# Optimization experiments

Hardware: AMD Instinct MI355X
Metric: run time of the kernel (lower is better)

Reference implementation:

```python
import jax, jax.numpy as jnp
import numpy as np
from jax import lax

H, W = 64, 64          # image_shape grid
TOP_K = 3
N_ITER = 50
EPS = 1e-8
NPTS = 3072            # N = M feature points (<= H*W)
SQRT2 = 1.4142135623730951
INV_SQRT3 = 1.0 / 1.7320508075688772


def setup_inputs() -> dict:
    key = jax.random.key(0)
    P = jax.random.uniform(key, (NPTS + 1, NPTS + 1), dtype=jnp.float32)
    K = jnp.array([[500.0, 0.0, 320.0],
                   [0.0, 500.0, 240.0],
                   [0.0, 0.0, 1.0]], dtype=jnp.float32)
    return {"P": P, "K": K}


def _power_iter(Mm, v0):
    # n_iter steps of v <- Mm @ v / ||.||  (differentiable via scan)
    def step(v, _):
        v = Mm @ v
        return v / (jnp.linalg.norm(v) + EPS), None
    v, _ = lax.scan(step, v0, None, length=N_ITER)
    return v


def _det3(M):
    return (M[0, 0] * (M[1, 1] * M[2, 2] - M[1, 2] * M[2, 1])
            - M[0, 1] * (M[1, 0] * M[2, 2] - M[1, 2] * M[2, 0])
            + M[0, 2] * (M[1, 0] * M[2, 1] - M[1, 1] * M[2, 0]))


def _hartley(pts, w):
    # weighted centroid + scale so weighted RMS distance = sqrt(2)
    ws = w.sum() + EPS
    c = (w[:, None] * pts).sum(0) / ws
    pc = pts - c
    md = jnp.sqrt((w * (pc ** 2).sum(-1)).sum() / ws + EPS)
    s = jnp.asarray(SQRT2, pts.dtype) / (md + EPS)
    z = jnp.zeros((), pts.dtype)
    o = jnp.ones((), pts.dtype)
    T = jnp.stack([jnp.stack([s, z, -s * c[0]]),
                   jnp.stack([z, s, -s * c[1]]),
                   jnp.stack([z, z, o])])
    return T, s, c


def _project_E(E):
    # project onto essential manifold: singular values -> [s, s, 0]
    B = E.T @ E
    lam = jnp.trace(B)
    v0 = jnp.full((3,), INV_SQRT3, E.dtype)
    v1 = _power_iter(B, v0)                                   # max eigvec of E^T E
    v3 = _power_iter(lam * jnp.eye(3, dtype=E.dtype) - B, v0)  # min eigvec
    v2 = jnp.cross(v3, v1)
    v2 = v2 / (jnp.linalg.norm(v2) + EPS)
    V = jnp.stack([v1, v2, v3], axis=-1)
    one = jnp.ones((), E.dtype)
    sV = jnp.sign(_det3(V))
    V = V * jnp.stack([one, one, sV])[None, :]
    Ev1 = E @ V[:, 0]
    Ev2 = E @ V[:, 1]
    s1 = jnp.linalg.norm(Ev1)
    s2 = jnp.linalg.norm(Ev2)
    s_avg = (s1 + s2) / 2.0
    u1 = Ev1 / (s1 + EPS)
    u2 = Ev2 / (s2 + EPS)
    u3 = jnp.cross(u1, u2)
    U = jnp.stack([u1, u2, u3], axis=-1)
    sU = jnp.sign(_det3(U))
    U = U * jnp.stack([one, one, sU])[None, :]
    z = jnp.zeros((), E.dtype)
    # U @ diag(s_avg, s_avg, 0) @ V^T, diag folded into column scaling
    return (U * jnp.stack([s_avg, s_avg, z])[None, :]) @ V.T


def reference(P, K):
    N = P.shape[0] - 1
    M = P.shape[1] - 1
    Pc = P[:N, :M]
    # bidirectional top-k + absolute threshold
    tr = lax.top_k(Pc, TOP_K)[0][:, TOP_K - 1]          # (N,) row thresholds
    tc = lax.top_k(Pc.T, TOP_K)[0][:, TOP_K - 1]        # (M,) col thresholds
    mask = (Pc >= tr[:, None]) & (Pc >= tc[None, :]) & (Pc > 0.01)
    weights = Pc * mask.astype(Pc.dtype)
    # grid pixel coords -> normalized camera coords via K^-1
    idx = jnp.arange(H * W, dtype=Pc.dtype)
    pix = jnp.stack([idx % W, jnp.floor(idx / W)], axis=-1)  # (HW, 2)
    K_inv = jnp.linalg.inv(K)
    p1h = jnp.concatenate([pix[:N], jnp.ones((N, 1), Pc.dtype)], axis=-1)
    p2h = jnp.concatenate([pix[:M], jnp.ones((M, 1), Pc.dtype)], axis=-1)
    pts1 = (p1h @ K_inv.T)[:, :2]
    pts2 = (p2h @ K_inv.T)[:, :2]
    w1 = weights.sum(1)
    w2 = weights.sum(0)
    T1, s1, c1 = _hartley(pts1, w1)
    T2, s2, c2 = _hartley(pts2, w2)
    p1 = (pts1 - c1) * s1
    p2 = (pts2 - c2) * s2
    x1, y1 = p1[:, 0], p1[:, 1]
    x2, y2 = p2[:, 0], p2[:, 1]
    on = jnp.ones((N,), Pc.dtype)
    om = jnp.ones((M,), Pc.dtype)
    # (N, M, 9) epipolar design matrix
    A = jnp.stack([x1[:, None] * x2[None, :], x1[:, None] * y2[None, :], x1[:, None] * om[None, :],
                   y1[:, None] * x2[None, :], y1[:, None] * y2[None, :], y1[:, None] * om[None, :],
                   on[:, None] * x2[None, :], on[:, None] * y2[None, :], jnp.ones((N, M), Pc.dtype)],
                  axis=-1)
    A9 = A.reshape(N * M, 9)
    Mmat = (A9 * weights.reshape(-1, 1)).T @ A9            # 9x9 weighted Gram
    # min eigenvector via shifted power iteration
    lam = jnp.trace(Mmat)
    Ms = lam * jnp.eye(9, dtype=Mmat.dtype) - Mmat
    v = _power_iter(Ms, jnp.full((9,), 1.0 / 3.0, Mmat.dtype))
    E_raw = v.reshape(3, 3)
    E = T2.T @ E_raw @ T1                                   # Hartley denormalize
    return _project_E(E)
```

## Files before the change

### kernel.cpp

```cpp
#include <hip/hip_runtime.h>
#include <math.h>

#define NPV 3072
#define LDP 3073
#define EPSF 1e-8f
#define NMOM 52
#define NROWBLK (NPV / 64)

#define INS3(v, a, b, c) do { \
    float _m1 = fminf((a), (v)); (a) = fmaxf((a), (v)); \
    float _m2 = fminf((b), _m1); (b) = fmaxf((b), _m1); \
    (c) = fmaxf((c), _m2); } while (0)

#define MRG3(x, y, z, a, b, c) do { \
    INS3((x), a, b, c); INS3((y), a, b, c); INS3((z), a, b, c); } while (0)

__device__ __forceinline__ void kinv6(const float* __restrict__ Kmat,
        float& ki0, float& ki1, float& ki2, float& ki3, float& ki4, float& ki5)
{
    float k00 = Kmat[0], k01 = Kmat[1], k02 = Kmat[2];
    float k10 = Kmat[3], k11 = Kmat[4], k12 = Kmat[5];
    float k20 = Kmat[6], k21 = Kmat[7], k22 = Kmat[8];
    float det = k00 * (k11 * k22 - k12 * k21) - k01 * (k10 * k22 - k12 * k20) + k02 * (k10 * k21 - k11 * k20);
    float id = 1.0f / det;
    ki0 = (k11 * k22 - k12 * k21) * id; ki1 = (k02 * k21 - k01 * k22) * id; ki2 = (k01 * k12 - k02 * k11) * id;
    ki3 = (k12 * k20 - k10 * k22) * id; ki4 = (k00 * k22 - k02 * k20) * id; ki5 = (k02 * k10 - k00 * k12) * id;
}

__global__ __launch_bounds__(256) void k_row_top3(const float* __restrict__ P,
        float* __restrict__ tr, int* __restrict__ rowcnt)
{
    int lane = threadIdx.x & 63;
    int i = blockIdx.x * 4 + (threadIdx.x >> 6);
    const float* row = P + (size_t)i * LDP;
    float a0 = -1e30f, b0 = -1e30f, c0 = -1e30f;
    float a1 = -1e30f, b1 = -1e30f, c1 = -1e30f;
    float a2 = -1e30f, b2 = -1e30f, c2 = -1e30f;
    float a3 = -1e30f, b3 = -1e30f, c3 = -1e30f;
    #pragma unroll
    for (int r = 0; r < 48; r += 4) {
        float v0 = row[(r + 0) * 64 + lane];
        float v1 = row[(r + 1) * 64 + lane];
        float v2 = row[(r + 2) * 64 + lane];
        float v3 = row[(r + 3) * 64 + lane];
        INS3(v0, a0, b0, c0);
        INS3(v1, a1, b1, c1);
        INS3(v2, a2, b2, c2);
        INS3(v3, a3, b3, c3);
    }
    MRG3(a1, b1, c1, a0, b0, c0);
    MRG3(a2, b2, c2, a0, b0, c0);
    MRG3(a3, b3, c3, a0, b0, c0);
    #pragma unroll
    for (int off = 1; off < 64; off <<= 1) {
        float xa = __shfl_xor(a0, off);
        float xb = __shfl_xor(b0, off);
        float xc = __shfl_xor(c0, off);
        MRG3(xa, xb, xc, a0, b0, c0);
    }
    if (lane == 0) { tr[i] = c0; rowcnt[i] = 0; }
}

#define CAND(v, i) do { \
    if ((v) >= tr[i] && (v) > 0.01f) { \
        int _s = atomicAdd(&rowcnt[i], 1); \
        if (_s < 8) { rowj[(size_t)(i) * 8 + _s] = j; roww[(size_t)(i) * 8 + _s] = (v); } \
    } } while (0)

__global__ __launch_bounds__(256) void k_col_pass(const float* __restrict__ P,
        const float* __restrict__ tr, float4* __restrict__ part, int segrows,
        int* __restrict__ rowcnt, int* __restrict__ rowj, float* __restrict__ roww)
{
    int j = blockIdx.x * 256 + threadIdx.x;
    int i0 = blockIdx.y * segrows;
    float a0 = -1e30f, b0 = -1e30f, c0 = -1e30f;
    float a1 = -1e30f, b1 = -1e30f, c1 = -1e30f;
    float a2 = -1e30f, b2 = -1e30f, c2 = -1e30f;
    float a3 = -1e30f, b3 = -1e30f, c3 = -1e30f;
    float a4 = -1e30f, b4 = -1e30f, c4 = -1e30f;
    float a5 = -1e30f, b5 = -1e30f, c5 = -1e30f;
    float a6 = -1e30f, b6 = -1e30f, c6 = -1e30f;
    float a7 = -1e30f, b7 = -1e30f, c7 = -1e30f;
    for (int r = 0; r < segrows; r += 8) {
        int i = i0 + r;
        const float* col = P + (size_t)i * LDP + j;
        float v0 = col[0 * LDP];
        float v1 = col[1 * LDP];
        float v2 = col[2 * LDP];
        float v3 = col[3 * LDP];
        float v4 = col[4 * LDP];
        float v5 = col[5 * LDP];
        float v6 = col[6 * LDP];
        float v7 = col[7 * LDP];
        INS3(v0, a0, b0, c0);
        INS3(v1, a1, b1, c1);
        INS3(v2, a2, b2, c2);
        INS3(v3, a3, b3, c3);
        INS3(v4, a4, b4, c4);
        INS3(v5, a5, b5, c5);
        INS3(v6, a6, b6, c6);
        INS3(v7, a7, b7, c7);
        CAND(v0, i + 0);
        CAND(v1, i + 1);
        CAND(v2, i + 2);
        CAND(v3, i + 3);
        CAND(v4, i + 4);
        CAND(v5, i + 5);
        CAND(v6, i + 6);
        CAND(v7, i + 7);
    }
    MRG3(a1, b1, c1, a0, b0, c0);
    MRG3(a2, b2, c2, a0, b0, c0);
    MRG3(a3, b3, c3, a0, b0, c0);
    MRG3(a4, b4, c4, a0, b0, c0);
    MRG3(a5, b5, c5, a0, b0, c0);
    MRG3(a6, b6, c6, a0, b0, c0);
    MRG3(a7, b7, c7, a0, b0, c0);
    part[(size_t)blockIdx.y * NPV + j] = make_float4(a0, b0, c0, 0.f);
}

template<int NSEG>
__global__ __launch_bounds__(256) void k_col_merge(const float4* __restrict__ part,
        float* __restrict__ tc)
{
    int sub = threadIdx.x & 15;
    int j = blockIdx.x * 16 + (threadIdx.x >> 4);
    constexpr int CNT = NSEG / 16;
    float4 buf[CNT];
    #pragma unroll
    for (int k = 0; k < CNT; ++k)
        buf[k] = part[(size_t)(sub + (k << 4)) * NPV + j];
    float a = -1e30f, b = -1e30f, c = -1e30f;
    #pragma unroll
    for (int k = 0; k < CNT; ++k) MRG3(buf[k].x, buf[k].y, buf[k].z, a, b, c);
    #pragma unroll
    for (int off = 1; off < 16; off <<= 1) {
        float xa = __shfl_xor(a, off);
        float xb = __shfl_xor(b, off);
        float xc = __shfl_xor(c, off);
        MRG3(xa, xb, xc, a, b, c);
    }
    if (sub == 0) tc[j] = c;
}

__device__ __forceinline__ void acc_pair(float* m, float w, float xs1, float ys1,
                                         float xs2, float ys2)
{
    m[0] += w;
    m[1] += w * xs1; m[2] += w * ys1; m[3] += w * (xs1 * xs1 + ys1 * ys1);
    m[4] += w * xs2; m[5] += w * ys2; m[6] += w * (xs2 * xs2 + ys2 * ys2);
    float a[9] = { xs1 * xs2, xs1 * ys2, xs1, ys1 * xs2, ys1 * ys2, ys1, xs2, ys2, 1.f };
    int idx = 7;
    #pragma unroll
    for (int u = 0; u < 9; ++u) {
        float wa = w * a[u];
        #pragma unroll
        for (int v = u; v < 9; ++v) { m[idx] = fmaf(wa, a[v], m[idx]); ++idx; }
    }
}

__global__ __launch_bounds__(64) void k_moments(const float* __restrict__ Kmat,
        const float* __restrict__ tc, const int* __restrict__ rowcnt,
        const int* __restrict__ rowj, const float* __restrict__ roww,
        float* __restrict__ momp)
{
    int i = blockIdx.x * 64 + threadIdx.x;
    float ki0, ki1, ki2, ki3, ki4, ki5;
    kinv6(Kmat, ki0, ki1, ki2, ki3, ki4, ki5);
    float m[NMOM];
    #pragma unroll
    for (int k = 0; k < NMOM; ++k) m[k] = 0.f;
    int n = rowcnt[i]; n = n > 8 ? 8 : n;
    const int4*   jp = (const int4*)(rowj + (size_t)i * 8);
    const float4* vp = (const float4*)(roww + (size_t)i * 8);
    int4  ja = jp[0], jb = jp[1];
    float4 va = vp[0], vb = vp[1];
    float xg = (float)(i & 63) - 31.5f, yg = (float)(i >> 6) - 23.5f;
    float xs1 = ki0 * xg + ki1 * yg;
    float ys1 = ki3 * xg + ki4 * yg;
#define ACC(S, JR, VR) do { \
    if ((S) < n) { int _j = (JR); float _w = (VR); \
        if (_w >= tc[_j]) { \
            float _xg = (float)(_j & 63) - 31.5f, _yg = (float)(_j >> 6) - 23.5f; \
            float xs2 = ki0 * _xg + ki1 * _yg; \
            float ys2 = ki3 * _xg + ki4 * _yg; \
            acc_pair(m, _w, xs1, ys1, xs2, ys2); \
        } } } while (0)
    ACC(0, ja.x, va.x); ACC(1, ja.y, va.y); ACC(2, ja.z, va.z); ACC(3, ja.w, va.w);
    ACC(4, jb.x, vb.x); ACC(5, jb.y, vb.y); ACC(6, jb.z, vb.z); ACC(7, jb.w, vb.w);
#undef ACC
    #pragma unroll
    for (int k = 0; k < NMOM; ++k) {
        #pragma unroll
        for (int off = 32; off; off >>= 1) m[k] += __shfl_xor(m[k], off);
    }
    if (threadIdx.x == 0) {
        float* dst = momp + (size_t)blockIdx.x * 64;
        #pragma unroll
        for (int k = 0; k < NMOM; ++k) dst[k] = m[k];
    }
}

__device__ __forceinline__ void mm3r(const float* A, const float* B, float* C) {
    #pragma unroll
    for (int r = 0; r < 3; ++r)
        #pragma unroll
        for (int c = 0; c < 3; ++c)
            C[r * 3 + c] = A[r * 3 + 0] * B[0 + c] + A[r * 3 + 1] * B[3 + c] + A[r * 3 + 2] * B[6 + c];
}

__device__ __forceinline__ float det3(const float* M) {
    return M[0] * (M[4] * M[8] - M[5] * M[7])
         - M[1] * (M[3] * M[8] - M[5] * M[6])
         + M[2] * (M[3] * M[7] - M[4] * M[6]);
}

__global__ __launch_bounds__(128) void k_tail(const float* __restrict__ Kmat,
        const float* __restrict__ momp, float* __restrict__ out)
{
    __shared__ float sMom[NMOM];
    __shared__ float sM[81], sY[81], sP[81], sT[81];
    __shared__ float sT1[9], sT2[9];
    int t = threadIdx.x;

    if (t < NMOM) {
        float s = 0.f;
        for (int b = 0; b < NROWBLK; ++b) s += momp[(size_t)b * 64 + t];
        sMom[t] = s;
    }
    __syncthreads();

    float ki0, ki1, ki2, ki3, ki4, ki5;
    kinv6(Kmat, ki0, ki1, ki2, ki3, ki4, ki5);
    float u0x = ki0 * 31.5f + ki1 * 23.5f + ki2;
    float u0y = ki3 * 31.5f + ki4 * 23.5f + ki5;

    float Sw = sMom[0];
    float ws = Sw + EPSF;
    float c1x = sMom[1] / ws, c1y = sMom[2] / ws;
    float c2x = sMom[4] / ws, c2y = sMom[5] / ws;
    float q1 = (sMom[3] - 2.f * (c1x * sMom[1] + c1y * sMom[2]) + (c1x * c1x + c1y * c1y) * Sw) / ws;
    float q2 = (sMom[6] - 2.f * (c2x * sMom[4] + c2y * sMom[5]) + (c2x * c2x + c2y * c2y) * Sw) / ws;
    float md1 = sqrtf(fmaxf(q1, 0.f) + EPSF);
    float md2 = sqrtf(fmaxf(q2, 0.f) + EPSF);
    float s1 = 1.4142135623730951f / (md1 + EPSF);
    float s2 = 1.4142135623730951f / (md2 + EPSF);

    if (t < 81) {
        int r = t / 9, c = t % 9;
        int u = r < c ? r : c, v = r < c ? c : r;
        int idx = 7 + u * 9 - (u * (u + 1)) / 2 + v;
        sM[t] = sMom[idx];
    }
    if (t == 0) {
        sT1[0] = s1; sT1[1] = 0.f; sT1[2] = -s1 * c1x;
        sT1[3] = 0.f; sT1[4] = s1; sT1[5] = -s1 * c1y;
        sT1[6] = 0.f; sT1[7] = 0.f; sT1[8] = 1.f;
        sT2[0] = s2; sT2[1] = 0.f; sT2[2] = -s2 * c2x;
        sT2[3] = 0.f; sT2[4] = s2; sT2[5] = -s2 * c2y;
        sT2[6] = 0.f; sT2[7] = 0.f; sT2[8] = 1.f;
    }
    __syncthreads();

    if (t < 81) {
        int k = t / 9, c = t % 9;
        float s = 0.f;
        #pragma unroll
        for (int l = 0; l < 9; ++l)
            s = fmaf(sM[k * 9 + l], sT1[(c / 3) * 3 + (l / 3)] * sT2[(c % 3) * 3 + (l % 3)], s);
        sY[t] = s;
    }
    __syncthreads();
    if (t < 81) {
        int r = t / 9, c = t % 9;
        float s = 0.f;
        #pragma unroll
        for (int k = 0; k < 9; ++k)
            s = fmaf(sT1[(r / 3) * 3 + (k / 3)] * sT2[(r % 3) * 3 + (k % 3)], sY[k * 9 + c], s);
        sP[t] = s;
    }
    __syncthreads();
    if (t < 81) {
        int r = t / 9, c = t % 9;
        float lam = sP[0] + sP[10] + sP[20] + sP[30] + sP[40] + sP[50] + sP[60] + sP[70] + sP[80];
        float il = 1.f / (lam + 1e-30f);
        sM[t] = ((r == c ? lam : 0.f) - sP[t]) * il;
    }
    __syncthreads();

#define MM81(DST, A, B) \
    if (t < 81) { \
        int _r = t / 9, _c = t % 9; \
        float _s = 0.f; \
        _Pragma("unroll") \
        for (int _k = 0; _k < 9; ++_k) _s = fmaf(A[_r * 9 + _k], B[_k * 9 + _c], _s); \
        DST[t] = _s; \
    } \
    __syncthreads();

    MM81(sY, sM, sM)
    MM81(sP, sY, sY)
    MM81(sT, sP, sP)
    MM81(sP, sT, sT)
    MM81(sT, sP, sP)
    MM81(sM, sT, sP)
    MM81(sT, sM, sY)

    if (t < 64) {
        float v9[9];
        float nrm = 0.f;
        #pragma unroll
        for (int r = 0; r < 9; ++r) {
            float s = 0.f;
            #pragma unroll
            for (int c = 0; c < 9; ++c) s += sT[r * 9 + c];
            v9[r] = s * (1.f / 3.f);
            nrm += v9[r] * v9[r];
        }
        nrm = sqrtf(nrm) + EPSF;
        #pragma unroll
        for (int r = 0; r < 9; ++r) v9[r] /= nrm;

        float C1x = c1x + u0x, C1y = c1y + u0y;
        float C2x = c2x + u0x, C2y = c2y + u0y;
        float T1f[9] = { s1, 0.f, -s1 * C1x, 0.f, s1, -s1 * C1y, 0.f, 0.f, 1.f };
        float T2t[9] = { s2, 0.f, 0.f, 0.f, s2, 0.f, -s2 * C2x, -s2 * C2y, 1.f };
        float M1[9], Ee[9];
        mm3r(v9, T1f, M1);
        mm3r(T2t, M1, Ee);

        float B[9];
        #pragma unroll
        for (int r = 0; r < 3; ++r)
            #pragma unroll
            for (int c = 0; c < 3; ++c)
                B[r * 3 + c] = Ee[r] * Ee[c] + Ee[3 + r] * Ee[3 + c] + Ee[6 + r] * Ee[6 + c];
        float lam3 = B[0] + B[4] + B[8];
        float il3 = 1.f / (lam3 + 1e-30f);

        int parity = t & 1;
        float P1[9];
        #pragma unroll
        for (int k = 0; k < 9; ++k) {
            float d = (k == 0 || k == 4 || k == 8) ? lam3 : 0.f;
            P1[k] = (parity ? (d - B[k]) : B[k]) * il3;
        }
        float P2[9], P4[9], P8[9], P16[9], P32[9], R1[9], P50[9];
        mm3r(P1, P1, P2);
        mm3r(P2, P2, P4);
        mm3r(P4, P4, P8);
        mm3r(P8, P8, P16);
        mm3r(P16, P16, P32);
        mm3r(P32, P16, R1);
        mm3r(R1, P2, P50);
        float vx = (P50[0] + P50[1] + P50[2]) * 0.57735026918962584f;
        float vy = (P50[3] + P50[4] + P50[5]) * 0.57735026918962584f;
        float vz = (P50[6] + P50[7] + P50[8]) * 0.57735026918962584f;
        float vn = sqrtf(vx * vx + vy * vy + vz * vz) + EPSF;
        vx /= vn; vy /= vn; vz /= vn;

        float v3x = __shfl(vx, 1), v3y = __shfl(vy, 1), v3z = __shfl(vz, 1);

        if (t == 0) {
            float v1[3] = { vx, vy, vz };
            float v3[3] = { v3x, v3y, v3z };
            float v2[3];
            v2[0] = v3[1] * v1[2] - v3[2] * v1[1];
            v2[1] = v3[2] * v1[0] - v3[0] * v1[2];
            v2[2] = v3[0] * v1[1] - v3[1] * v1[0];
            float n2 = sqrtf(v2[0] * v2[0] + v2[1] * v2[1] + v2[2] * v2[2]) + EPSF;
            v2[0] /= n2; v2[1] /= n2; v2[2] /= n2;
            float V[9];
            #pragma unroll
            for (int r = 0; r < 3; ++r) { V[r * 3 + 0] = v1[r]; V[r * 3 + 1] = v2[r]; V[r * 3 + 2] = v3[r]; }
            float dV = det3(V);
            float sV = (dV > 0.f) ? 1.f : ((dV < 0.f) ? -1.f : 0.f);
            V[2] *= sV; V[5] *= sV; V[8] *= sV;
            float Ev1[3], Ev2[3];
            #pragma unroll
            for (int r = 0; r < 3; ++r) {
                Ev1[r] = Ee[r * 3] * V[0] + Ee[r * 3 + 1] * V[3] + Ee[r * 3 + 2] * V[6];
                Ev2[r] = Ee[r * 3] * V[1] + Ee[r * 3 + 1] * V[4] + Ee[r * 3 + 2] * V[7];
            }
            float s1n = sqrtf(Ev1[0] * Ev1[0] + Ev1[1] * Ev1[1] + Ev1[2] * Ev1[2]);
            float s2n = sqrtf(Ev2[0] * Ev2[0] + Ev2[1] * Ev2[1] + Ev2[2] * Ev2[2]);
            float s_avg = (s1n + s2n) * 0.5f;
            float u1[3], u2[3];
            #pragma unroll
            for (int r = 0; r < 3; ++r) { u1[r] = Ev1[r] / (s1n + EPSF); u2[r] = Ev2[r] / (s2n + EPSF); }
            #pragma unroll
            for (int r = 0; r < 3; ++r)
                #pragma unroll
                for (int c = 0; c < 3; ++c)
                    out[r * 3 + c] = s_avg * (u1[r] * V[c * 3 + 0] + u2[r] * V[c * 3 + 1]);
        }
    }
}

extern "C" void kernel_launch(void* const* d_in, const int* in_sizes, int n_in,
                              void* d_out, int out_size, void* d_ws, size_t ws_size,
                              hipStream_t stream)
{
    const float* P = (const float*)d_in[0];
    const float* K = (const float*)d_in[1];
    float* out = (float*)d_out;

    float* fws    = (float*)d_ws;
    float* tr     = fws;
    float* tc     = tr + NPV;
    float* roww   = tc + NPV;
    int*   rowj   = (int*)(roww + 8 * NPV);
    int*   rowcnt = rowj + 8 * NPV;
    float* momp   = (float*)(rowcnt + NPV);
    float4* part  = (float4*)(momp + NROWBLK * 64);

    size_t fixed_bytes = ((size_t)NPV * 19 + NROWBLK * 64) * sizeof(float);
    int nseg = 16;
    for (int cand = 128; cand >= 16; cand >>= 1) {
        if (ws_size >= fixed_bytes + (size_t)cand * NPV * sizeof(float4)) { nseg = cand; break; }
    }
    int segrows = NPV / nseg;

    k_row_top3<<<NPV / 4, 256, 0, stream>>>(P, tr, rowcnt);
    dim3 g2(NPV / 256, nseg);
    k_col_pass<<<g2, 256, 0, stream>>>(P, tr, part, segrows, rowcnt, rowj, roww);
    switch (nseg) {
        case 128: k_col_merge<128><<<NPV / 16, 256, 0, stream>>>(part, tc); break;
        case 64:  k_col_merge<64><<<NPV / 16, 256, 0, stream>>>(part, tc); break;
        case 32:  k_col_merge<32><<<NPV / 16, 256, 0, stream>>>(part, tc); break;
        default:  k_col_merge<16><<<NPV / 16, 256, 0, stream>>>(part, tc); break;
    }
    k_moments<<<NPV / 64, 64, 0, stream>>>(K, tc, rowcnt, rowj, roww, momp);
    k_tail<<<1, 128, 0, stream>>>(K, momp, out);
}
```

Before: 38.34 us.

## Fuse row top-3 with candidate selection and moments, drop atomic candidate lists

The separate row top-3 kernel and the atomic candidate scatter inside the column pass are removed. A new row kernel computes the row top-3, tests candidates against the column threshold using wave ballots into shared memory, and accumulates the moments in the same pass. The tail kernel now reduces 768 partial blocks with 1024 threads. This trades one full read of P plus the atomics for a second row-major read of P after the column merge. Each row is capped at 24 candidates where it was capped at 8 before.

```diff
diff --git a/kernel.cpp b/kernel.cpp
--- a/kernel.cpp
+++ b/kernel.cpp
@@ -5,7 +5,8 @@
 #define LDP 3073
 #define EPSF 1e-8f
 #define NMOM 52
-#define NROWBLK (NPV / 64)
+#define NBLK 768
+#define CAP 24
 
 #define INS3(v, a, b, c) do { \
     float _m1 = fminf((a), (v)); (a) = fmaxf((a), (v)); \
@@ -27,49 +28,8 @@
     ki3 = (k12 * k20 - k10 * k22) * id; ki4 = (k00 * k22 - k02 * k20) * id; ki5 = (k02 * k10 - k00 * k12) * id;
 }
 
-__global__ __launch_bounds__(256) void k_row_top3(const float* __restrict__ P,
-        float* __restrict__ tr, int* __restrict__ rowcnt)
-{
-    int lane = threadIdx.x & 63;
-    int i = blockIdx.x * 4 + (threadIdx.x >> 6);
-    const float* row = P + (size_t)i * LDP;
-    float a0 = -1e30f, b0 = -1e30f, c0 = -1e30f;
-    float a1 = -1e30f, b1 = -1e30f, c1 = -1e30f;
-    float a2 = -1e30f, b2 = -1e30f, c2 = -1e30f;
-    float a3 = -1e30f, b3 = -1e30f, c3 = -1e30f;
-    #pragma unroll
-    for (int r = 0; r < 48; r += 4) {
-        float v0 = row[(r + 0) * 64 + lane];
-        float v1 = row[(r + 1) * 64 + lane];
-        float v2 = row[(r + 2) * 64 + lane];
-        float v3 = row[(r + 3) * 64 + lane];
-        INS3(v0, a0, b0, c0);
-        INS3(v1, a1, b1, c1);
-        INS3(v2, a2, b2, c2);
-        INS3(v3, a3, b3, c3);
-    }
-    MRG3(a1, b1, c1, a0, b0, c0);
-    MRG3(a2, b2, c2, a0, b0, c0);
-    MRG3(a3, b3, c3, a0, b0, c0);
-    #pragma unroll
-    for (int off = 1; off < 64; off <<= 1) {
-        float xa = __shfl_xor(a0, off);
-        float xb = __shfl_xor(b0, off);
-        float xc = __shfl_xor(c0, off);
-        MRG3(xa, xb, xc, a0, b0, c0);
-    }
-    if (lane == 0) { tr[i] = c0; rowcnt[i] = 0; }
-}
-
-#define CAND(v, i) do { \
-    if ((v) >= tr[i] && (v) > 0.01f) { \
-        int _s = atomicAdd(&rowcnt[i], 1); \
-        if (_s < 8) { rowj[(size_t)(i) * 8 + _s] = j; roww[(size_t)(i) * 8 + _s] = (v); } \
-    } } while (0)
-
 __global__ __launch_bounds__(256) void k_col_pass(const float* __restrict__ P,
-        const float* __restrict__ tr, float4* __restrict__ part, int segrows,
-        int* __restrict__ rowcnt, int* __restrict__ rowj, float* __restrict__ roww)
+        float4* __restrict__ part, int segrows)
 {
     int j = blockIdx.x * 256 + threadIdx.x;
     int i0 = blockIdx.y * segrows;
@@ -82,8 +42,7 @@
     float a6 = -1e30f, b6 = -1e30f, c6 = -1e30f;
     float a7 = -1e30f, b7 = -1e30f, c7 = -1e30f;
     for (int r = 0; r < segrows; r += 8) {
-        int i = i0 + r;
-        const float* col = P + (size_t)i * LDP + j;
+        const float* col = P + (size_t)(i0 + r) * LDP + j;
         float v0 = col[0 * LDP];
         float v1 = col[1 * LDP];
         float v2 = col[2 * LDP];
@@ -100,14 +59,6 @@
         INS3(v5, a5, b5, c5);
         INS3(v6, a6, b6, c6);
         INS3(v7, a7, b7, c7);
-        CAND(v0, i + 0);
-        CAND(v1, i + 1);
-        CAND(v2, i + 2);
-        CAND(v3, i + 3);
-        CAND(v4, i + 4);
-        CAND(v5, i + 5);
-        CAND(v6, i + 6);
-        CAND(v7, i + 7);
     }
     MRG3(a1, b1, c1, a0, b0, c0);
     MRG3(a2, b2, c2, a0, b0, c0);
@@ -159,46 +110,99 @@
     }
 }
 
-__global__ __launch_bounds__(64) void k_moments(const float* __restrict__ Kmat,
-        const float* __restrict__ tc, const int* __restrict__ rowcnt,
-        const int* __restrict__ rowj, const float* __restrict__ roww,
+__global__ __launch_bounds__(256) void k_row_mom(const float* __restrict__ P,
+        const float* __restrict__ tc, const float* __restrict__ Kmat,
         float* __restrict__ momp)
 {
-    int i = blockIdx.x * 64 + threadIdx.x;
+    __shared__ int   jsl[4][CAP];
+    __shared__ float vsl[4][CAP];
+    __shared__ float sPart[4][NMOM];
+    int lane = threadIdx.x & 63;
+    int wid  = threadIdx.x >> 6;
+    int i = blockIdx.x * 4 + wid;
+    const float* row = P + (size_t)i * LDP;
+    unsigned long long ltm = (1ull << lane) - 1ull;
+
+    float a0 = -1e30f, b0 = -1e30f, c0 = -1e30f;
+    float a1 = -1e30f, b1 = -1e30f, c1 = -1e30f;
+    float a2 = -1e30f, b2 = -1e30f, c2 = -1e30f;
+    float a3 = -1e30f, b3 = -1e30f, c3 = -1e30f;
+    int cnt = 0;
+
+#define CTEST(vk, tk, jk) do { \
+        bool _p = ((vk) >= (tk)) && ((vk) > 0.01f); \
+        unsigned long long _m = __ballot(_p); \
+        if (_p) { \
+            int _pos = cnt + (int)__popcll(_m & ltm); \
+            if (_pos < CAP) { jsl[wid][_pos] = (jk); vsl[wid][_pos] = (vk); } \
+        } \
+        cnt += (int)__popcll(_m); } while (0)
+
+    #pragma unroll
+    for (int r = 0; r < 48; r += 4) {
+        float v0 = row[(r + 0) * 64 + lane];
+        float v1 = row[(r + 1) * 64 + lane];
+        float v2 = row[(r + 2) * 64 + lane];
+        float v3 = row[(r + 3) * 64 + lane];
+        float t0 = tc[(r + 0) * 64 + lane];
+        float t1 = tc[(r + 1) * 64 + lane];
+        float t2 = tc[(r + 2) * 64 + lane];
+        float t3 = tc[(r + 3) * 64 + lane];
+        INS3(v0, a0, b0, c0);
+        INS3(v1, a1, b1, c1);
+        INS3(v2, a2, b2, c2);
+        INS3(v3, a3, b3, c3);
+        CTEST(v0, t0, (r + 0) * 64 + lane);
+        CTEST(v1, t1, (r + 1) * 64 + lane);
+        CTEST(v2, t2, (r + 2) * 64 + lane);
+        CTEST(v3, t3, (r + 3) * 64 + lane);
+    }
+#undef CTEST
+    MRG3(a1, b1, c1, a0, b0, c0);
+    MRG3(a2, b2, c2, a0, b0, c0);
+    MRG3(a3, b3, c3, a0, b0, c0);
+    #pragma unroll
+    for (int off = 1; off < 64; off <<= 1) {
+        float xa = __shfl_xor(a0, off);
+        float xb = __shfl_xor(b0, off);
+        float xc = __shfl_xor(c0, off);
+        MRG3(xa, xb, xc, a0, b0, c0);
+    }
+
     float ki0, ki1, ki2, ki3, ki4, ki5;
     kinv6(Kmat, ki0, ki1, ki2, ki3, ki4, ki5);
-    float m[NMOM];
-    #pragma unroll
-    for (int k = 0; k < NMOM; ++k) m[k] = 0.f;
-    int n = rowcnt[i]; n = n > 8 ? 8 : n;
-    const int4*   jp = (const int4*)(rowj + (size_t)i * 8);
-    const float4* vp = (const float4*)(roww + (size_t)i * 8);
-    int4  ja = jp[0], jb = jp[1];
-    float4 va = vp[0], vb = vp[1];
-    float xg = (float)(i & 63) - 31.5f, yg = (float)(i >> 6) - 23.5f;
-    float xs1 = ki0 * xg + ki1 * yg;
-    float ys1 = ki3 * xg + ki4 * yg;
-#define ACC(S, JR, VR) do { \
-    if ((S) < n) { int _j = (JR); float _w = (VR); \
-        if (_w >= tc[_j]) { \
-            float _xg = (float)(_j & 63) - 31.5f, _yg = (float)(_j >> 6) - 23.5f; \
-            float xs2 = ki0 * _xg + ki1 * _yg; \
-            float ys2 = ki3 * _xg + ki4 * _yg; \
-            acc_pair(m, _w, xs1, ys1, xs2, ys2); \
-        } } } while (0)
-    ACC(0, ja.x, va.x); ACC(1, ja.y, va.y); ACC(2, ja.z, va.z); ACC(3, ja.w, va.w);
-    ACC(4, jb.x, vb.x); ACC(5, jb.y, vb.y); ACC(6, jb.z, vb.z); ACC(7, jb.w, vb.w);
-#undef ACC
+
+    float mloc[NMOM];
+    #pragma unroll
+    for (int k = 0; k < NMOM; ++k) mloc[k] = 0.f;
+    int n = cnt < CAP ? cnt : CAP;
+    if (lane < n) {
+        int j = jsl[wid][lane];
+        float w = vsl[wid][lane];
+        if (w >= c0) {
+            float xg = (float)(i & 63) - 31.5f, yg = (float)(i >> 6) - 23.5f;
+            float xs1 = ki0 * xg + ki1 * yg;
+            float ys1 = ki3 * xg + ki4 * yg;
+            float xj = (float)(j & 63) - 31.5f, yj = (float)(j >> 6) - 23.5f;
+            float xs2 = ki0 * xj + ki1 * yj;
+            float ys2 = ki3 * xj + ki4 * yj;
+            acc_pair(mloc, w, xs1, ys1, xs2, ys2);
+        }
+    }
     #pragma unroll
     for (int k = 0; k < NMOM; ++k) {
         #pragma unroll
-        for (int off = 32; off; off >>= 1) m[k] += __shfl_xor(m[k], off);
-    }
-    if (threadIdx.x == 0) {
-        float* dst = momp + (size_t)blockIdx.x * 64;
-        #pragma unroll
-        for (int k = 0; k < NMOM; ++k) dst[k] = m[k];
-    }
+        for (int off = 32; off; off >>= 1) mloc[k] += __shfl_xor(mloc[k], off);
+    }
+    if (lane == 0) {
+        #pragma unroll
+        for (int k = 0; k < NMOM; ++k) sPart[wid][k] = mloc[k];
+    }
+    __syncthreads();
+    if (threadIdx.x < NMOM)
+        momp[(size_t)blockIdx.x * 64 + threadIdx.x] =
+            sPart[0][threadIdx.x] + sPart[1][threadIdx.x] +
+            sPart[2][threadIdx.x] + sPart[3][threadIdx.x];
 }
 
 __device__ __forceinline__ void mm3r(const float* A, const float* B, float* C) {
@@ -215,17 +219,28 @@
          + M[2] * (M[3] * M[7] - M[4] * M[6]);
 }
 
-__global__ __launch_bounds__(128) void k_tail(const float* __restrict__ Kmat,
+__global__ __launch_bounds__(1024) void k_tail(const float* __restrict__ Kmat,
         const float* __restrict__ momp, float* __restrict__ out)
 {
+    __shared__ float sRed[16][64];
     __shared__ float sMom[NMOM];
     __shared__ float sM[81], sY[81], sP[81], sT[81];
     __shared__ float sT1[9], sT2[9];
     int t = threadIdx.x;
 
+    {
+        int c = t >> 6, k = t & 63;
+        float s = 0.f;
+        #pragma unroll 8
+        for (int p = 0; p < NBLK / 16; ++p)
+            s += momp[(size_t)(c * (NBLK / 16) + p) * 64 + k];
+        sRed[c][k] = s;
+    }
+    __syncthreads();
     if (t < NMOM) {
         float s = 0.f;
-        for (int b = 0; b < NROWBLK; ++b) s += momp[(size_t)b * 64 + t];
+        #pragma unroll
+        for (int c = 0; c < 16; ++c) s += sRed[c][t];
         sMom[t] = s;
     }
     __syncthreads();
@@ -405,31 +420,26 @@
     const float* K = (const float*)d_in[1];
     float* out = (float*)d_out;
 
-    float* fws    = (float*)d_ws;
-    float* tr     = fws;
-    float* tc     = tr + NPV;
-    float* roww   = tc + NPV;
-    int*   rowj   = (int*)(roww + 8 * NPV);
-    int*   rowcnt = rowj + 8 * NPV;
-    float* momp   = (float*)(rowcnt + NPV);
-    float4* part  = (float4*)(momp + NROWBLK * 64);
-
-    size_t fixed_bytes = ((size_t)NPV * 19 + NROWBLK * 64) * sizeof(float);
+    float* fws   = (float*)d_ws;
+    float* tc    = fws;
+    float* momp  = tc + NPV;
+    float4* part = (float4*)(momp + NBLK * 64);
+
+    size_t fixed_bytes = ((size_t)NPV + NBLK * 64) * sizeof(float);
     int nseg = 16;
     for (int cand = 128; cand >= 16; cand >>= 1) {
         if (ws_size >= fixed_bytes + (size_t)cand * NPV * sizeof(float4)) { nseg = cand; break; }
     }
     int segrows = NPV / nseg;
 
-    k_row_top3<<<NPV / 4, 256, 0, stream>>>(P, tr, rowcnt);
-    dim3 g2(NPV / 256, nseg);
-    k_col_pass<<<g2, 256, 0, stream>>>(P, tr, part, segrows, rowcnt, rowj, roww);
+    dim3 g1(NPV / 256, nseg);
+    k_col_pass<<<g1, 256, 0, stream>>>(P, part, segrows);
     switch (nseg) {
         case 128: k_col_merge<128><<<NPV / 16, 256, 0, stream>>>(part, tc); break;
         case 64:  k_col_merge<64><<<NPV / 16, 256, 0, stream>>>(part, tc); break;
         case 32:  k_col_merge<32><<<NPV / 16, 256, 0, stream>>>(part, tc); break;
         default:  k_col_merge<16><<<NPV / 16, 256, 0, stream>>>(part, tc); break;
     }
-    k_moments<<<NPV / 64, 64, 0, stream>>>(K, tc, rowcnt, rowj, roww, momp);
-    k_tail<<<1, 128, 0, stream>>>(K, momp, out);
-}
+    k_row_mom<<<NBLK, 256, 0, stream>>>(P, tc, K, momp);
+    k_tail<<<1, 1024, 0, stream>>>(K, momp, out);
+}
```

After: 45.42 us. 1.18x slower.

## Fuse row and column top-3 into one tiled pass with LDS transpose

Applied to the files above, without the earlier changes.

Replaces the separate row-top3 kernel and the atomic candidate gathering with a single tiled kernel. Each tile reads a 48x256 block of P once, computes the column partial top-3 in registers and the per-row top-3 (with indices) by staging the tile through LDS. A new row-merge kernel combines the per-chunk row top-3 results and accumulates moments, and the last-arriving block (ticket counter) runs the tail, so the separate tail launch is gone. The intent is to read P once instead of twice and to drop two launches and the atomics. In exchange it adds LDS traffic, a serial 256-wide row scan done by only 48 threads per block, and a fixed segment count.

```diff
diff --git a/kernel.cpp b/kernel.cpp
--- a/kernel.cpp
+++ b/kernel.cpp
@@ -5,7 +5,11 @@
 #define LDP 3073
 #define EPSF 1e-8f
 #define NMOM 52
-#define NROWBLK (NPV / 64)
+#define NSEG 64
+#define NCHUNK 12
+#define NTILE (NSEG * NCHUNK)
+#define NMOMBLK 12
+#define NPART (NMOMBLK * 4)
 
 #define INS3(v, a, b, c) do { \
     float _m1 = fminf((a), (v)); (a) = fmaxf((a), (v)); \
@@ -14,6 +18,19 @@
 
 #define MRG3(x, y, z, a, b, c) do { \
     INS3((x), a, b, c); INS3((y), a, b, c); INS3((z), a, b, c); } while (0)
+
+#define INSJ(v, j, a, ja, b, jb, c, jc) do { \
+    bool _g1 = (v) > (a); \
+    bool _g2 = (v) > (b); \
+    bool _g3 = (v) > (c); \
+    float _nc = _g2 ? (b) : (_g3 ? (v) : (c)); \
+    int  _njc = _g2 ? (jb) : (_g3 ? (j) : (jc)); \
+    float _nb = _g1 ? (a) : (_g2 ? (v) : (b)); \
+    int  _njb = _g1 ? (ja) : (_g2 ? (j) : (jb)); \
+    (a) = _g1 ? (v) : (a); \
+    (ja) = _g1 ? (j) : (ja); \
+    (b) = _nb; (jb) = _njb; \
+    (c) = _nc; (jc) = _njc; } while (0)
 
 __device__ __forceinline__ void kinv6(const float* __restrict__ Kmat,
         float& ki0, float& ki1, float& ki2, float& ki3, float& ki4, float& ki5)
@@ -27,52 +44,17 @@
     ki3 = (k12 * k20 - k10 * k22) * id; ki4 = (k00 * k22 - k02 * k20) * id; ki5 = (k02 * k10 - k00 * k12) * id;
 }
 
-__global__ __launch_bounds__(256) void k_row_top3(const float* __restrict__ P,
-        float* __restrict__ tr, int* __restrict__ rowcnt)
-{
-    int lane = threadIdx.x & 63;
-    int i = blockIdx.x * 4 + (threadIdx.x >> 6);
-    const float* row = P + (size_t)i * LDP;
-    float a0 = -1e30f, b0 = -1e30f, c0 = -1e30f;
-    float a1 = -1e30f, b1 = -1e30f, c1 = -1e30f;
-    float a2 = -1e30f, b2 = -1e30f, c2 = -1e30f;
-    float a3 = -1e30f, b3 = -1e30f, c3 = -1e30f;
-    #pragma unroll
-    for (int r = 0; r < 48; r += 4) {
-        float v0 = row[(r + 0) * 64 + lane];
-        float v1 = row[(r + 1) * 64 + lane];
-        float v2 = row[(r + 2) * 64 + lane];
-        float v3 = row[(r + 3) * 64 + lane];
-        INS3(v0, a0, b0, c0);
-        INS3(v1, a1, b1, c1);
-        INS3(v2, a2, b2, c2);
-        INS3(v3, a3, b3, c3);
-    }
-    MRG3(a1, b1, c1, a0, b0, c0);
-    MRG3(a2, b2, c2, a0, b0, c0);
-    MRG3(a3, b3, c3, a0, b0, c0);
-    #pragma unroll
-    for (int off = 1; off < 64; off <<= 1) {
-        float xa = __shfl_xor(a0, off);
-        float xb = __shfl_xor(b0, off);
-        float xc = __shfl_xor(c0, off);
-        MRG3(xa, xb, xc, a0, b0, c0);
-    }
-    if (lane == 0) { tr[i] = c0; rowcnt[i] = 0; }
-}
-
-#define CAND(v, i) do { \
-    if ((v) >= tr[i] && (v) > 0.01f) { \
-        int _s = atomicAdd(&rowcnt[i], 1); \
-        if (_s < 8) { rowj[(size_t)(i) * 8 + _s] = j; roww[(size_t)(i) * 8 + _s] = (v); } \
-    } } while (0)
-
-__global__ __launch_bounds__(256) void k_col_pass(const float* __restrict__ P,
-        const float* __restrict__ tr, float4* __restrict__ part, int segrows,
-        int* __restrict__ rowcnt, int* __restrict__ rowj, float* __restrict__ roww)
-{
-    int j = blockIdx.x * 256 + threadIdx.x;
-    int i0 = blockIdx.y * segrows;
+__global__ __launch_bounds__(256) void k_tile(const float* __restrict__ P,
+        float4* __restrict__ part, float* __restrict__ rpv, int* __restrict__ rpj)
+{
+    __shared__ float lds[48][257];
+    int t = threadIdx.x;
+    int chunk = blockIdx.x % NCHUNK;
+    int seg   = blockIdx.x / NCHUNK;
+    int j0 = chunk * 256;
+    int i0 = seg * 48;
+    const float* base = P + (size_t)i0 * LDP + j0 + t;
+
     float a0 = -1e30f, b0 = -1e30f, c0 = -1e30f;
     float a1 = -1e30f, b1 = -1e30f, c1 = -1e30f;
     float a2 = -1e30f, b2 = -1e30f, c2 = -1e30f;
@@ -81,17 +63,24 @@
     float a5 = -1e30f, b5 = -1e30f, c5 = -1e30f;
     float a6 = -1e30f, b6 = -1e30f, c6 = -1e30f;
     float a7 = -1e30f, b7 = -1e30f, c7 = -1e30f;
-    for (int r = 0; r < segrows; r += 8) {
-        int i = i0 + r;
-        const float* col = P + (size_t)i * LDP + j;
-        float v0 = col[0 * LDP];
-        float v1 = col[1 * LDP];
-        float v2 = col[2 * LDP];
-        float v3 = col[3 * LDP];
-        float v4 = col[4 * LDP];
-        float v5 = col[5 * LDP];
-        float v6 = col[6 * LDP];
-        float v7 = col[7 * LDP];
+    #pragma unroll
+    for (int r = 0; r < 48; r += 8) {
+        float v0 = base[(size_t)(r + 0) * LDP];
+        float v1 = base[(size_t)(r + 1) * LDP];
+        float v2 = base[(size_t)(r + 2) * LDP];
+        float v3 = base[(size_t)(r + 3) * LDP];
+        float v4 = base[(size_t)(r + 4) * LDP];
+        float v5 = base[(size_t)(r + 5) * LDP];
+        float v6 = base[(size_t)(r + 6) * LDP];
+        float v7 = base[(size_t)(r + 7) * LDP];
+        lds[r + 0][t] = v0;
+        lds[r + 1][t] = v1;
+        lds[r + 2][t] = v2;
+        lds[r + 3][t] = v3;
+        lds[r + 4][t] = v4;
+        lds[r + 5][t] = v5;
+        lds[r + 6][t] = v6;
+        lds[r + 7][t] = v7;
         INS3(v0, a0, b0, c0);
         INS3(v1, a1, b1, c1);
         INS3(v2, a2, b2, c2);
@@ -100,14 +89,6 @@
         INS3(v5, a5, b5, c5);
         INS3(v6, a6, b6, c6);
         INS3(v7, a7, b7, c7);
-        CAND(v0, i + 0);
-        CAND(v1, i + 1);
-        CAND(v2, i + 2);
-        CAND(v3, i + 3);
-        CAND(v4, i + 4);
-        CAND(v5, i + 5);
-        CAND(v6, i + 6);
-        CAND(v7, i + 7);
     }
     MRG3(a1, b1, c1, a0, b0, c0);
     MRG3(a2, b2, c2, a0, b0, c0);
@@ -116,23 +97,58 @@
     MRG3(a5, b5, c5, a0, b0, c0);
     MRG3(a6, b6, c6, a0, b0, c0);
     MRG3(a7, b7, c7, a0, b0, c0);
-    part[(size_t)blockIdx.y * NPV + j] = make_float4(a0, b0, c0, 0.f);
-}
-
-template<int NSEG>
-__global__ __launch_bounds__(256) void k_col_merge(const float4* __restrict__ part,
-        float* __restrict__ tc)
-{
+    part[(size_t)seg * NPV + j0 + t] = make_float4(a0, b0, c0, 0.f);
+
+    __syncthreads();
+
+    if (t < 48) {
+        float A0 = -1e30f, B0 = -1e30f, C0 = -1e30f; int JA0 = 0, JB0 = 0, JC0 = 0;
+        float A1 = -1e30f, B1 = -1e30f, C1 = -1e30f; int JA1 = 0, JB1 = 0, JC1 = 0;
+        float A2 = -1e30f, B2 = -1e30f, C2 = -1e30f; int JA2 = 0, JB2 = 0, JC2 = 0;
+        float A3 = -1e30f, B3 = -1e30f, C3 = -1e30f; int JA3 = 0, JB3 = 0, JC3 = 0;
+        #pragma unroll 8
+        for (int s = 0; s < 256; s += 4) {
+            float v0 = lds[t][s + 0];
+            float v1 = lds[t][s + 1];
+            float v2 = lds[t][s + 2];
+            float v3 = lds[t][s + 3];
+            INSJ(v0, j0 + s + 0, A0, JA0, B0, JB0, C0, JC0);
+            INSJ(v1, j0 + s + 1, A1, JA1, B1, JB1, C1, JC1);
+            INSJ(v2, j0 + s + 2, A2, JA2, B2, JB2, C2, JC2);
+            INSJ(v3, j0 + s + 3, A3, JA3, B3, JB3, C3, JC3);
+        }
+        INSJ(A1, JA1, A0, JA0, B0, JB0, C0, JC0);
+        INSJ(B1, JB1, A0, JA0, B0, JB0, C0, JC0);
+        INSJ(C1, JC1, A0, JA0, B0, JB0, C0, JC0);
+        INSJ(A2, JA2, A0, JA0, B0, JB0, C0, JC0);
+        INSJ(B2, JB2, A0, JA0, B0, JB0, C0, JC0);
+        INSJ(C2, JC2, A0, JA0, B0, JB0, C0, JC0);
+        INSJ(A3, JA3, A0, JA0, B0, JB0, C0, JC0);
+        INSJ(B3, JB3, A0, JA0, B0, JB0, C0, JC0);
+        INSJ(C3, JC3, A0, JA0, B0, JB0, C0, JC0);
+        int i = i0 + t;
+        rpv[(chunk * 3 + 0) * NPV + i] = A0;
+        rpv[(chunk * 3 + 1) * NPV + i] = B0;
+        rpv[(chunk * 3 + 2) * NPV + i] = C0;
+        rpj[(chunk * 3 + 0) * NPV + i] = JA0;
+        rpj[(chunk * 3 + 1) * NPV + i] = JB0;
+        rpj[(chunk * 3 + 2) * NPV + i] = JC0;
+    }
+}
+
+__global__ __launch_bounds__(256) void k_colmerge(const float4* __restrict__ part,
+        float* __restrict__ tc, int* __restrict__ ticket)
+{
+    if (blockIdx.x == 0 && threadIdx.x == 0) *ticket = 0;
     int sub = threadIdx.x & 15;
     int j = blockIdx.x * 16 + (threadIdx.x >> 4);
-    constexpr int CNT = NSEG / 16;
-    float4 buf[CNT];
-    #pragma unroll
-    for (int k = 0; k < CNT; ++k)
+    float4 buf[NSEG / 16];
+    #pragma unroll
+    for (int k = 0; k < NSEG / 16; ++k)
         buf[k] = part[(size_t)(sub + (k << 4)) * NPV + j];
     float a = -1e30f, b = -1e30f, c = -1e30f;
     #pragma unroll
-    for (int k = 0; k < CNT; ++k) MRG3(buf[k].x, buf[k].y, buf[k].z, a, b, c);
+    for (int k = 0; k < NSEG / 16; ++k) MRG3(buf[k].x, buf[k].y, buf[k].z, a, b, c);
     #pragma unroll
     for (int off = 1; off < 16; off <<= 1) {
         float xa = __shfl_xor(a, off);
@@ -159,48 +175,6 @@
     }
 }
 
-__global__ __launch_bounds__(64) void k_moments(const float* __restrict__ Kmat,
-        const float* __restrict__ tc, const int* __restrict__ rowcnt,
-        const int* __restrict__ rowj, const float* __restrict__ roww,
-        float* __restrict__ momp)
-{
-    int i = blockIdx.x * 64 + threadIdx.x;
-    float ki0, ki1, ki2, ki3, ki4, ki5;
-    kinv6(Kmat, ki0, ki1, ki2, ki3, ki4, ki5);
-    float m[NMOM];
-    #pragma unroll
-    for (int k = 0; k < NMOM; ++k) m[k] = 0.f;
-    int n = rowcnt[i]; n = n > 8 ? 8 : n;
-    const int4*   jp = (const int4*)(rowj + (size_t)i * 8);
-    const float4* vp = (const float4*)(roww + (size_t)i * 8);
-    int4  ja = jp[0], jb = jp[1];
-    float4 va = vp[0], vb = vp[1];
-    float xg = (float)(i & 63) - 31.5f, yg = (float)(i >> 6) - 23.5f;
-    float xs1 = ki0 * xg + ki1 * yg;
-    float ys1 = ki3 * xg + ki4 * yg;
-#define ACC(S, JR, VR) do { \
-    if ((S) < n) { int _j = (JR); float _w = (VR); \
-        if (_w >= tc[_j]) { \
-            float _xg = (float)(_j & 63) - 31.5f, _yg = (float)(_j >> 6) - 23.5f; \
-            float xs2 = ki0 * _xg + ki1 * _yg; \
-            float ys2 = ki3 * _xg + ki4 * _yg; \
-            acc_pair(m, _w, xs1, ys1, xs2, ys2); \
-        } } } while (0)
-    ACC(0, ja.x, va.x); ACC(1, ja.y, va.y); ACC(2, ja.z, va.z); ACC(3, ja.w, va.w);
-    ACC(4, jb.x, vb.x); ACC(5, jb.y, vb.y); ACC(6, jb.z, vb.z); ACC(7, jb.w, vb.w);
-#undef ACC
-    #pragma unroll
-    for (int k = 0; k < NMOM; ++k) {
-        #pragma unroll
-        for (int off = 32; off; off >>= 1) m[k] += __shfl_xor(m[k], off);
-    }
-    if (threadIdx.x == 0) {
-        float* dst = momp + (size_t)blockIdx.x * 64;
-        #pragma unroll
-        for (int k = 0; k < NMOM; ++k) dst[k] = m[k];
-    }
-}
-
 __device__ __forceinline__ void mm3r(const float* A, const float* B, float* C) {
     #pragma unroll
     for (int r = 0; r < 3; ++r)
@@ -215,17 +189,17 @@
          + M[2] * (M[3] * M[7] - M[4] * M[6]);
 }
 
-__global__ __launch_bounds__(128) void k_tail(const float* __restrict__ Kmat,
-        const float* __restrict__ momp, float* __restrict__ out)
+__device__ void ph_tail(const float* __restrict__ Kmat,
+        const float* __restrict__ momp, float* __restrict__ out, int t)
 {
     __shared__ float sMom[NMOM];
     __shared__ float sM[81], sY[81], sP[81], sT[81];
     __shared__ float sT1[9], sT2[9];
-    int t = threadIdx.x;
 
     if (t < NMOM) {
         float s = 0.f;
-        for (int b = 0; b < NROWBLK; ++b) s += momp[(size_t)b * 64 + t];
+        #pragma unroll 8
+        for (int b = 0; b < NPART; ++b) s += momp[(size_t)b * 64 + t];
         sMom[t] = s;
     }
     __syncthreads();
@@ -305,6 +279,7 @@
     MM81(sT, sP, sP)
     MM81(sM, sT, sP)
     MM81(sT, sM, sY)
+#undef MM81
 
     if (t < 64) {
         float v9[9];
@@ -397,6 +372,68 @@
     }
 }
 
+__global__ __launch_bounds__(256) void k_rowmom(const float* __restrict__ Kmat,
+        const float* __restrict__ tc, const float* __restrict__ rpv,
+        const int* __restrict__ rpj, float* __restrict__ momp,
+        int* __restrict__ ticket, float* __restrict__ out)
+{
+    __shared__ int slast;
+    int t = threadIdx.x;
+    int i = blockIdx.x * 256 + t;
+
+    float A = -1e30f, B = -1e30f, C = -1e30f;
+    int JA = 0, JB = 0, JC = 0;
+    #pragma unroll
+    for (int ch = 0; ch < NCHUNK; ++ch) {
+        #pragma unroll
+        for (int k = 0; k < 3; ++k) {
+            float v = rpv[(size_t)(ch * 3 + k) * NPV + i];
+            int   j = rpj[(size_t)(ch * 3 + k) * NPV + i];
+            INSJ(v, j, A, JA, B, JB, C, JC);
+        }
+    }
+
+    float ki0, ki1, ki2, ki3, ki4, ki5;
+    kinv6(Kmat, ki0, ki1, ki2, ki3, ki4, ki5);
+    float m[NMOM];
+    #pragma unroll
+    for (int k = 0; k < NMOM; ++k) m[k] = 0.f;
+    float xg = (float)(i & 63) - 31.5f, yg = (float)(i >> 6) - 23.5f;
+    float xs1 = ki0 * xg + ki1 * yg;
+    float ys1 = ki3 * xg + ki4 * yg;
+#define ACCJ(V, J) do { \
+    if ((V) > 0.01f && (V) >= tc[J]) { \
+        float _xg = (float)((J) & 63) - 31.5f, _yg = (float)((J) >> 6) - 23.5f; \
+        float xs2 = ki0 * _xg + ki1 * _yg; \
+        float ys2 = ki3 * _xg + ki4 * _yg; \
+        acc_pair(m, (V), xs1, ys1, xs2, ys2); \
+    } } while (0)
+    ACCJ(A, JA);
+    ACCJ(B, JB);
+    ACCJ(C, JC);
+#undef ACCJ
+
+    #pragma unroll
+    for (int k = 0; k < NMOM; ++k) {
+        #pragma unroll
+        for (int off = 32; off; off >>= 1) m[k] += __shfl_xor(m[k], off);
+    }
+    int lane = t & 63, wid = t >> 6;
+    if (lane == 0) {
+        float* dst = momp + (size_t)(blockIdx.x * 4 + wid) * 64;
+        #pragma unroll
+        for (int k = 0; k < NMOM; ++k) dst[k] = m[k];
+    }
+
+    __threadfence();
+    __syncthreads();
+    if (t == 0) slast = (atomicAdd(ticket, 1) == NMOMBLK - 1) ? 1 : 0;
+    __syncthreads();
+    if (!slast) return;
+    __threadfence();
+    ph_tail(Kmat, momp, out, t);
+}
+
 extern "C" void kernel_launch(void* const* d_in, const int* in_sizes, int n_in,
                               void* d_out, int out_size, void* d_ws, size_t ws_size,
                               hipStream_t stream)
@@ -405,31 +442,15 @@
     const float* K = (const float*)d_in[1];
     float* out = (float*)d_out;
 
-    float* fws    = (float*)d_ws;
-    float* tr     = fws;
-    float* tc     = tr + NPV;
-    float* roww   = tc + NPV;
-    int*   rowj   = (int*)(roww + 8 * NPV);
-    int*   rowcnt = rowj + 8 * NPV;
-    float* momp   = (float*)(rowcnt + NPV);
-    float4* part  = (float4*)(momp + NROWBLK * 64);
-
-    size_t fixed_bytes = ((size_t)NPV * 19 + NROWBLK * 64) * sizeof(float);
-    int nseg = 16;
-    for (int cand = 128; cand >= 16; cand >>= 1) {
-        if (ws_size >= fixed_bytes + (size_t)cand * NPV * sizeof(float4)) { nseg = cand; break; }
-    }
-    int segrows = NPV / nseg;
-
-    k_row_top3<<<NPV / 4, 256, 0, stream>>>(P, tr, rowcnt);
-    dim3 g2(NPV / 256, nseg);
-    k_col_pass<<<g2, 256, 0, stream>>>(P, tr, part, segrows, rowcnt, rowj, roww);
-    switch (nseg) {
-        case 128: k_col_merge<128><<<NPV / 16, 256, 0, stream>>>(part, tc); break;
-        case 64:  k_col_merge<64><<<NPV / 16, 256, 0, stream>>>(part, tc); break;
-        case 32:  k_col_merge<32><<<NPV / 16, 256, 0, stream>>>(part, tc); break;
-        default:  k_col_merge<16><<<NPV / 16, 256, 0, stream>>>(part, tc); break;
-    }
-    k_moments<<<NPV / 64, 64, 0, stream>>>(K, tc, rowcnt, rowj, roww, momp);
-    k_tail<<<1, 128, 0, stream>>>(K, momp, out);
-}
+    float* fws   = (float*)d_ws;
+    float* tc    = fws;
+    float* rpv   = tc + NPV;
+    int*   rpj   = (int*)(rpv + 36 * NPV);
+    float* momp  = (float*)(rpj + 36 * NPV);
+    int*   ticket = (int*)(momp + NPART * 64);
+    float4* part = (float4*)(ticket + 16);
+
+    k_tile    <<<NTILE, 256, 0, stream>>>(P, part, rpv, rpj);
+    k_colmerge<<<NPV / 16, 256, 0, stream>>>(part, tc, ticket);
+    k_rowmom  <<<NMOMBLK, 256, 0, stream>>>(K, tc, rpv, rpj, momp, ticket, out);
+}
```

Result: slower. 44.52 us (+16.1%).
